# Kernel tuning notes

Measured on AMD Instinct MI355X. Metric: run time of the kernel, lower is better.

## Reference

```python
import jax, jax.numpy as jnp
import numpy as np

# ---- Mamba2 hyperparameters (from init_kwargs + mamba_ssm defaults) ----
D_MODEL = 1024
D_STATE = 64
D_CONV = 4
EXPAND = 2
HEADDIM = 64                       # mamba_ssm default
D_INNER = EXPAND * D_MODEL         # 2048
NHEADS = D_INNER // HEADDIM        # 32
CONV_DIM = D_INNER + 2 * D_STATE   # 2176 (ngroups=1)
D_IN_PROJ = 2 * D_INNER + 2 * D_STATE + NHEADS  # 4256
CHUNK = 64                         # SSD chunk length
EPS = 1e-5


def segsum(x):
    """Stable segment-sum: out[..., i, j] = sum_{k=j+1..i} x[..., k] for i>=j, else -inf."""
    T = x.shape[-1]
    cs = jnp.cumsum(x, axis=-1)
    ss = cs[..., :, None] - cs[..., None, :]
    mask = jnp.tril(jnp.ones((T, T), dtype=bool))
    return jnp.where(mask, ss, -jnp.inf)


def setup_inputs() -> dict:
    key = jax.random.key(0)
    ks = jax.random.split(key, 8)
    x = jax.random.normal(ks[0], (2, 2048, D_MODEL), dtype=jnp.float32)
    ln_w = jnp.ones((D_MODEL,), jnp.float32)
    ln_b = jnp.zeros((D_MODEL,), jnp.float32)
    in_proj_w = jax.random.normal(ks[1], (D_MODEL, D_IN_PROJ), jnp.float32) * 0.02
    conv_w = jax.random.normal(ks[2], (CONV_DIM, D_CONV), jnp.float32) * 0.2
    conv_b = jnp.zeros((CONV_DIM,), jnp.float32)
    dt_bias = jax.random.normal(ks[3], (NHEADS,), jnp.float32) * 0.5
    A_log = jnp.log(jax.random.uniform(ks[4], (NHEADS,), jnp.float32, 1.0, 16.0))
    D = jnp.ones((NHEADS,), jnp.float32)
    norm_w = jnp.ones((D_INNER,), jnp.float32)
    out_proj_w = jax.random.normal(ks[5], (D_INNER, D_MODEL), jnp.float32) * 0.02
    return {"x": x, "ln_w": ln_w, "ln_b": ln_b, "in_proj_w": in_proj_w,
            "conv_w": conv_w, "conv_b": conv_b, "dt_bias": dt_bias,
            "A_log": A_log, "D": D, "norm_w": norm_w, "out_proj_w": out_proj_w}


def reference(x, ln_w, ln_b, in_proj_w, conv_w, conv_b, dt_bias, A_log, D,
              norm_w, out_proj_w):
    b, l, _ = x.shape
    # ---- pre-norm (LayerNorm) ----
    mu = jnp.mean(x, -1, keepdims=True)
    var = jnp.mean((x - mu) ** 2, -1, keepdims=True)
    h = (x - mu) * jax.lax.rsqrt(var + EPS) * ln_w + ln_b

    # ---- input projection & split ----
    zxbcdt = h @ in_proj_w                                   # (b,l,4256)
    z, xBC, dt = jnp.split(zxbcdt, [D_INNER, D_INNER + CONV_DIM], axis=-1)

    # ---- causal depthwise conv1d + SiLU ----
    xp = jnp.pad(xBC, ((0, 0), (D_CONV - 1, 0), (0, 0)))
    xconv = sum(xp[:, k:k + l, :] * conv_w[:, k] for k in range(D_CONV)) + conv_b
    xBC = jax.nn.silu(xconv)
    xs, B, C = jnp.split(xBC, [D_INNER, D_INNER + D_STATE], axis=-1)

    dt = jax.nn.softplus(dt + dt_bias)                       # (b,l,h)
    A = -jnp.exp(A_log)                                      # (h,)
    X = xs.reshape(b, l, NHEADS, HEADDIM)                    # (b,l,h,p)

    # ---- SSD chunked selective scan ----
    c = l // CHUNK
    X_dt = X * dt[..., None]
    A_dt = dt * A                                            # (b,l,h)
    Xc = X_dt.reshape(b, c, CHUNK, NHEADS, HEADDIM)          # (b,c,T,h,p)
    Ac = A_dt.reshape(b, c, CHUNK, NHEADS).transpose(0, 3, 1, 2)  # (b,h,c,T)
    Bc = B.reshape(b, c, CHUNK, D_STATE)                     # (b,c,T,n)
    Cc = C.reshape(b, c, CHUNK, D_STATE)

    A_cs = jnp.cumsum(Ac, axis=-1)                           # (b,h,c,T)
    Lmat = jnp.exp(segsum(Ac))                               # (b,h,c,T,T)
    Y_diag = jnp.einsum("bcln,bcsn,bhcls,bcshp->bclhp", Cc, Bc, Lmat, Xc)

    decay_states = jnp.exp(A_cs[..., -1:] - A_cs)            # (b,h,c,T)
    states = jnp.einsum("bcln,bhcl,bclhp->bchpn", Bc, decay_states, Xc)

    A_last = jnp.pad(A_cs[..., -1], ((0, 0), (0, 0), (1, 0)))
    decay_chunk = jnp.exp(segsum(A_last))                    # (b,h,c+1,c+1)
    states = jnp.concatenate([jnp.zeros_like(states[:, :1]), states], axis=1)
    states = jnp.einsum("bhzc,bchpn->bzhpn", decay_chunk, states)[:, :-1]

    Y_off = jnp.einsum("bcln,bchpn,bhcl->bclhp", Cc, states, jnp.exp(A_cs))
    Y = (Y_diag + Y_off).reshape(b, l, NHEADS, HEADDIM)

    # ---- D skip, gated RMSNorm, output projection ----
    Y = Y + X * D[None, None, :, None]
    y = Y.reshape(b, l, D_INNER)
    y = y * jax.nn.silu(z)
    y = y * jax.lax.rsqrt(jnp.mean(y * y, -1, keepdims=True) + EPS) * norm_w
    out = y @ out_proj_w

    return x + out  # residual
```

## Files before the change

### kernel.cpp

```cpp
#include <hip/hip_runtime.h>
#include <hip/hip_bf16.h>

#define BATCH   2
#define SEQ     2048
#define DMODEL  1024
#define DINNER  2048
#define DSTATE  64
#define NHEADS  32
#define HEADDIM 64
#define CONVDIM 2176
#define DINPROJ 4256
#define NPAD    4352
#define NCHUNK  32
#define EPSF    1e-5f
#define SP      88
#define CDT     (CONVDIM + NHEADS)

typedef __bf16 bf16;
typedef bf16  bf16x4 __attribute__((ext_vector_type(4)));
typedef bf16  bf16x8 __attribute__((ext_vector_type(8)));
typedef float f32x4  __attribute__((ext_vector_type(4)));

__device__ __forceinline__ void gll16(const bf16* g, bf16* l) {
    __builtin_amdgcn_global_load_lds(
        (const __attribute__((address_space(1))) void*)g,
        (__attribute__((address_space(3))) void*)l, 16, 0, 0);
}

__global__ __launch_bounds__(256) void ln_kernel(
    const float* __restrict__ x, const float* __restrict__ w,
    const float* __restrict__ bv, bf16* __restrict__ h) {
    int row = blockIdx.x;
    const float* xr = x + (size_t)row * DMODEL;
    bf16* hr = h + (size_t)row * DMODEL;
    int t = threadIdx.x;
    float4 v = ((const float4*)xr)[t];
    float s  = v.x + v.y + v.z + v.w;
    float ss = v.x*v.x + v.y*v.y + v.z*v.z + v.w*v.w;
    for (int o = 32; o > 0; o >>= 1) { s += __shfl_down(s, o); ss += __shfl_down(ss, o); }
    __shared__ float red[2][4];
    int wid = t >> 6, lane = t & 63;
    if (lane == 0) { red[0][wid] = s; red[1][wid] = ss; }
    __syncthreads();
    if (t == 0) {
        float a = 0, b2 = 0;
        for (int i = 0; i < 4; i++) { a += red[0][i]; b2 += red[1][i]; }
        red[0][0] = a; red[1][0] = b2;
    }
    __syncthreads();
    float mean = red[0][0] * (1.f / DMODEL);
    float var  = red[1][0] * (1.f / DMODEL) - mean * mean;
    float rstd = rsqrtf(var + EPSF);
    for (int i = t; i < DMODEL; i += 256)
        hr[i] = (bf16)((xr[i] - mean) * rstd * w[i] + bv[i]);
}

__global__ __launch_bounds__(256) void cvt_w_both_kernel(
    const float* __restrict__ W1, const float* __restrict__ W2,
    bf16* __restrict__ Bt1, bf16* __restrict__ Bt2) {
    __shared__ float sm[32][33];
    int bid = blockIdx.x;
    const float* W; bf16* Bt; int K, N, NP, bx, by;
    if (bid < 4352) {
        W = W1; Bt = Bt1; K = 1024; N = 4256; NP = 4352;
        bx = bid % 136; by = bid / 136;
    } else {
        int b2 = bid - 4352;
        W = W2; Bt = Bt2; K = 2048; N = 1024; NP = 1024;
        bx = b2 % 32; by = b2 / 32;
    }
    int n0 = bx * 32, k0 = by * 32;
    int tx = threadIdx.x & 31, ty = threadIdx.x >> 5;
    for (int i = 0; i < 4; i++) {
        int k = k0 + ty + i * 8, n = n0 + tx;
        sm[ty + i * 8][tx] = (n < N) ? W[(size_t)k * N + n] : 0.f;
    }
    __syncthreads();
    for (int i = 0; i < 4; i++) {
        int n = n0 + ty + i * 8, k = k0 + tx;
        if (n < NP) Bt[(size_t)n * K + k] = (bf16)sm[tx][ty + i * 8];
    }
}

template<int BM, int BN, typename OUT_T>
__global__ __launch_bounds__(256) void gemm_bf16_pipe(
    const bf16* __restrict__ A, const bf16* __restrict__ Bt,
    OUT_T* __restrict__ C, int M, int N, int K,
    const float* __restrict__ resid) {
    constexpr int MR = BM / 32;
    constexpr int NR = BN / 32;
    __shared__ __align__(16) bf16 sA[2][BM * 32];
    __shared__ __align__(16) bf16 sB[2][BN * 32];
    int t = threadIdx.x;
    int lane = t & 63, w = t >> 6;
    int m0 = blockIdx.y * BM, n0 = blockIdx.x * BN;
    int wm = w >> 1, wn = w & 1;
    f32x4 acc[MR][NR] = {};
    int srow = w * 16 + (lane >> 2);
    int scol = (lane & 3) * 8;
    int fr = lane & 15;
    int fc = (lane >> 4) * 8;
    auto stage = [&](int buf, int k0) {
        #pragma unroll
        for (int i = 0; i < BM / 64; i++)
            gll16(&A[(size_t)(m0 + i * 64 + srow) * K + k0 + scol],
                  &sA[buf][(i * 64 + w * 16) * 32]);
        #pragma unroll
        for (int i = 0; i < BN / 64; i++)
            gll16(&Bt[(size_t)(n0 + i * 64 + srow) * K + k0 + scol],
                  &sB[buf][(i * 64 + w * 16) * 32]);
    };
    int nt = K / 32;
    stage(0, 0);
    __syncthreads();
    int cur = 0;
    for (int tt = 0; tt < nt; tt++) {
        if (tt + 1 < nt) stage(cur ^ 1, (tt + 1) * 32);
        bf16x8 af[MR], bfr[NR];
        #pragma unroll
        for (int i = 0; i < MR; i++)
            af[i] = *(const bf16x8*)&sA[cur][(wm * (BM/2) + i * 16 + fr) * 32 + fc];
        #pragma unroll
        for (int j = 0; j < NR; j++)
            bfr[j] = *(const bf16x8*)&sB[cur][(wn * (BN/2) + j * 16 + fr) * 32 + fc];
        #pragma unroll
        for (int i = 0; i < MR; i++)
            #pragma unroll
            for (int j = 0; j < NR; j++)
                acc[i][j] = __builtin_amdgcn_mfma_f32_16x16x32_bf16(
                    af[i], bfr[j], acc[i][j], 0, 0, 0);
        __syncthreads();
        cur ^= 1;
    }
    #pragma unroll
    for (int i = 0; i < MR; i++) {
        #pragma unroll
        for (int j = 0; j < NR; j++) {
            int col = n0 + wn * (BN/2) + j * 16 + (lane & 15);
            #pragma unroll
            for (int r = 0; r < 4; r++) {
                int row = m0 + wm * (BM/2) + i * 16 + (lane >> 4) * 4 + r;
                float v = acc[i][j][r];
                if (resid) v += resid[(size_t)row * N + col];
                C[(size_t)row * N + col] = (OUT_T)v;
            }
        }
    }
}

__global__ __launch_bounds__(256) void convdt_kernel(
    const bf16* __restrict__ zx, const float* __restrict__ cw,
    const float* __restrict__ cb, const float* __restrict__ dt_bias,
    bf16* __restrict__ xs, bf16* __restrict__ Bm, bf16* __restrict__ Cm,
    float* __restrict__ dtb) {
    int idx = blockIdx.x * 256 + threadIdx.x;
    int ch = idx % CDT;
    int bl = idx / CDT;
    if (ch >= CONVDIM) {
        int hh = ch - CONVDIM;
        float v = (float)zx[(size_t)bl * NPAD + DINNER + ch] + dt_bias[hh];
        dtb[bl * NHEADS + hh] = (v > 20.f) ? v : log1pf(expf(v));
        return;
    }
    int b = bl / SEQ, tt = bl % SEQ;
    float acc = cb[ch];
    #pragma unroll
    for (int k = 0; k < 4; k++) {
        int tp = tt - 3 + k;
        if (tp >= 0)
            acc += (float)zx[(size_t)(b * SEQ + tp) * NPAD + DINNER + ch] * cw[ch * 4 + k];
    }
    float s = acc / (1.f + expf(-acc));
    if (ch < DINNER)              xs[(size_t)bl * DINNER + ch] = (bf16)s;
    else if (ch < DINNER+DSTATE)  Bm[bl * DSTATE + (ch - DINNER)] = (bf16)s;
    else                          Cm[bl * DSTATE + (ch - DINNER - DSTATE)] = (bf16)s;
}

__global__ __launch_bounds__(256) void ssd_states_kernel(
    const bf16* __restrict__ xs, const bf16* __restrict__ Bm,
    const float* __restrict__ dtb, const float* __restrict__ A_log,
    bf16* __restrict__ states, float* __restrict__ Acs_g) {
    int blk = blockIdx.x;
    int hh = blk % NHEADS;
    int bc = blk / NHEADS;
    int c = bc % NCHUNK, b = bc / NCHUNK;
    __shared__ __align__(16) bf16 sXT[64 * SP];
    __shared__ __align__(16) bf16 sBT[64 * SP];
    __shared__ float dts[64], acs[64];
    int t = threadIdx.x;
    float Ah = -expf(A_log[hh]);
    if (t < 64) {
        float dv = dtb[(b * SEQ + c * 64 + t) * NHEADS + hh];
        float v = dv * Ah;
        #pragma unroll
        for (int o = 1; o < 64; o <<= 1) {
            float p = __shfl_up(v, o);
            if (t >= o) v += p;
        }
        dts[t] = dv; acs[t] = v;
        Acs_g[((b * NHEADS + hh) * NCHUNK + c) * 64 + t] = v;
    }
    __syncthreads();
    float alast = acs[63];
    {
        int l = t >> 2, c0 = (t & 3) * 16;
        int row = b * SEQ + c * 64 + l;
        float dl = dts[l];
        float wl = expf(alast - acs[l]);
        bf16x8 xv0 = *(const bf16x8*)&xs[(size_t)row * DINNER + hh * 64 + c0];
        bf16x8 xv1 = *(const bf16x8*)&xs[(size_t)row * DINNER + hh * 64 + c0 + 8];
        bf16x8 bv0 = *(const bf16x8*)&Bm[(size_t)row * DSTATE + c0];
        bf16x8 bv1 = *(const bf16x8*)&Bm[(size_t)row * DSTATE + c0 + 8];
        #pragma unroll
        for (int i = 0; i < 8; i++) {
            sXT[(c0 + i) * SP + l]     = (bf16)((float)xv0[i] * dl);
            sXT[(c0 + 8 + i) * SP + l] = (bf16)((float)xv1[i] * dl);
            sBT[(c0 + i) * SP + l]     = (bf16)((float)bv0[i] * wl);
            sBT[(c0 + 8 + i) * SP + l] = (bf16)((float)bv1[i] * wl);
        }
    }
    __syncthreads();
    int lane = t & 63, w = t >> 6;
    int wm = w >> 1, wn = w & 1;
    int fr = lane & 15, fc = (lane >> 4) * 8;
    f32x4 acc[2][2] = {};
    #pragma unroll
    for (int kk = 0; kk < 2; kk++) {
        bf16x8 a[2], bb[2];
        #pragma unroll
        for (int i = 0; i < 2; i++)
            a[i] = *(const bf16x8*)&sXT[(wm * 32 + i * 16 + fr) * SP + kk * 32 + fc];
        #pragma unroll
        for (int j = 0; j < 2; j++)
            bb[j] = *(const bf16x8*)&sBT[(wn * 32 + j * 16 + fr) * SP + kk * 32 + fc];
        #pragma unroll
        for (int i = 0; i < 2; i++)
            #pragma unroll
            for (int j = 0; j < 2; j++)
                acc[i][j] = __builtin_amdgcn_mfma_f32_16x16x32_bf16(
                    a[i], bb[j], acc[i][j], 0, 0, 0);
    }
    bf16* outp = states + (size_t)blk * 4096;
    #pragma unroll
    for (int i = 0; i < 2; i++)
        #pragma unroll
        for (int j = 0; j < 2; j++)
            #pragma unroll
            for (int r = 0; r < 4; r++)
                outp[(wm*32 + i*16 + (lane>>4)*4 + r) * 64 + wn*32 + j*16 + (lane&15)]
                    = (bf16)acc[i][j][r];
}

__global__ __launch_bounds__(256) void ssd_scan_kernel(
    bf16* __restrict__ states, const float* __restrict__ Acs_g) {
    int bid = blockIdx.x;
    int slice = bid & 3, bh = bid >> 2;
    int hh = bh % NHEADS, b = bh / NHEADS;
    int e0 = slice * 1024 + threadIdx.x * 4;
    bf16x4 loc[NCHUNK];
    float dec[NCHUNK];
    #pragma unroll
    for (int c = 0; c < NCHUNK; c++) {
        loc[c] = *(const bf16x4*)&states[(size_t)((b*NCHUNK+c)*NHEADS+hh)*4096 + e0];
        dec[c] = expf(Acs_g[((b*NHEADS+hh)*NCHUNK + c)*64 + 63]);
    }
    float S0 = 0.f, S1 = 0.f, S2 = 0.f, S3 = 0.f;
    #pragma unroll
    for (int c = 0; c < NCHUNK; c++) {
        bf16x4 l = loc[c];
        bf16x4 o; o[0] = (bf16)S0; o[1] = (bf16)S1; o[2] = (bf16)S2; o[3] = (bf16)S3;
        *(bf16x4*)&states[(size_t)((b*NCHUNK+c)*NHEADS+hh)*4096 + e0] = o;
        S0 = dec[c]*S0 + (float)l[0];
        S1 = dec[c]*S1 + (float)l[1];
        S2 = dec[c]*S2 + (float)l[2];
        S3 = dec[c]*S3 + (float)l[3];
    }
}

__global__ __launch_bounds__(256) void ssd_out_kernel(
    const bf16* __restrict__ xs, const bf16* __restrict__ Bm,
    const bf16* __restrict__ Cm, const float* __restrict__ dtb,
    const bf16* __restrict__ states, const float* __restrict__ Acs_g,
    const float* __restrict__ Dv, bf16* __restrict__ Y) {
    int blk = blockIdx.x;
    int hh = blk % NHEADS;
    int bc = blk / NHEADS;
    int c = bc % NCHUNK, b = bc / NCHUNK;
    __shared__ __align__(16) bf16 sC [64 * SP];
    __shared__ __align__(16) bf16 sBG[64 * SP];
    __shared__ __align__(16) bf16 sXS[64 * SP];
    __shared__ float acs[64], dts[64];
    int t = threadIdx.x;
    bf16x8 sreg0, sreg1;
    {
        const bf16* sp = states + (size_t)blk * 4096 + t * 16;
        sreg0 = *(const bf16x8*)&sp[0];
        sreg1 = *(const bf16x8*)&sp[8];
    }
    if (t < 64) {
        acs[t] = Acs_g[((b * NHEADS + hh) * NCHUNK + c) * 64 + t];
        dts[t] = dtb[(b * SEQ + c * 64 + t) * NHEADS + hh];
    }
    {
        int l = t >> 2, c0 = (t & 3) * 16;
        int row = b * SEQ + c * 64 + l;
        *(bf16x8*)&sC[l * SP + c0]      = *(const bf16x8*)&Cm[(size_t)row * DSTATE + c0];
        *(bf16x8*)&sC[l * SP + c0 + 8]  = *(const bf16x8*)&Cm[(size_t)row * DSTATE + c0 + 8];
        *(bf16x8*)&sBG[l * SP + c0]     = *(const bf16x8*)&Bm[(size_t)row * DSTATE + c0];
        *(bf16x8*)&sBG[l * SP + c0 + 8] = *(const bf16x8*)&Bm[(size_t)row * DSTATE + c0 + 8];
        bf16x8 xv0 = *(const bf16x8*)&xs[(size_t)row * DINNER + hh * 64 + c0];
        bf16x8 xv1 = *(const bf16x8*)&xs[(size_t)row * DINNER + hh * 64 + c0 + 8];
        #pragma unroll
        for (int i = 0; i < 8; i++) {
            sXS[(c0 + i) * SP + l]     = xv0[i];
            sXS[(c0 + 8 + i) * SP + l] = xv1[i];
        }
    }
    __syncthreads();
    int lane = t & 63, w = t >> 6;
    int wm = w >> 1, wn = w & 1;
    int fr = lane & 15, fc = (lane >> 4) * 8;
    f32x4 g[2][2] = {};
    #pragma unroll
    for (int kk = 0; kk < 2; kk++) {
        bf16x8 a[2], bb[2];
        #pragma unroll
        for (int i = 0; i < 2; i++)
            a[i] = *(const bf16x8*)&sC[(wm * 32 + i * 16 + fr) * SP + kk * 32 + fc];
        #pragma unroll
        for (int j = 0; j < 2; j++)
            bb[j] = *(const bf16x8*)&sBG[(wn * 32 + j * 16 + fr) * SP + kk * 32 + fc];
        #pragma unroll
        for (int i = 0; i < 2; i++)
            #pragma unroll
            for (int j = 0; j < 2; j++)
                g[i][j] = __builtin_amdgcn_mfma_f32_16x16x32_bf16(a[i], bb[j], g[i][j], 0, 0, 0);
    }
    __syncthreads();
    #pragma unroll
    for (int i = 0; i < 2; i++) {
        #pragma unroll
        for (int j = 0; j < 2; j++) {
            int s = wn * 32 + j * 16 + (lane & 15);
            #pragma unroll
            for (int r = 0; r < 4; r++) {
                int l = wm * 32 + i * 16 + (lane >> 4) * 4 + r;
                float val = (s <= l) ? g[i][j][r] * expf(acs[l] - acs[s]) * dts[s] : 0.f;
                sBG[l * SP + s] = (bf16)val;
            }
        }
    }
    __syncthreads();
    f32x4 yd[2][2] = {};
    #pragma unroll
    for (int kk = 0; kk < 2; kk++) {
        bf16x8 a[2], bb[2];
        #pragma unroll
        for (int i = 0; i < 2; i++)
            a[i] = *(const bf16x8*)&sBG[(wm * 32 + i * 16 + fr) * SP + kk * 32 + fc];
        #pragma unroll
        for (int j = 0; j < 2; j++)
            bb[j] = *(const bf16x8*)&sXS[(wn * 32 + j * 16 + fr) * SP + kk * 32 + fc];
        #pragma unroll
        for (int i = 0; i < 2; i++)
            #pragma unroll
            for (int j = 0; j < 2; j++)
                yd[i][j] = __builtin_amdgcn_mfma_f32_16x16x32_bf16(a[i], bb[j], yd[i][j], 0, 0, 0);
    }
    float xk[2][2][4];
    #pragma unroll
    for (int i = 0; i < 2; i++)
        #pragma unroll
        for (int j = 0; j < 2; j++) {
            int p = wn * 32 + j * 16 + (lane & 15);
            #pragma unroll
            for (int r = 0; r < 4; r++) {
                int l = wm * 32 + i * 16 + (lane >> 4) * 4 + r;
                xk[i][j][r] = (float)sXS[p * SP + l];
            }
        }
    __syncthreads();
    {
        int p = t >> 2, n0 = (t & 3) * 16;
        *(bf16x8*)&sXS[p * SP + n0]     = sreg0;
        *(bf16x8*)&sXS[p * SP + n0 + 8] = sreg1;
    }
    __syncthreads();
    f32x4 yo[2][2] = {};
    #pragma unroll
    for (int kk = 0; kk < 2; kk++) {
        bf16x8 a[2], bb[2];
        #pragma unroll
        for (int i = 0; i < 2; i++)
            a[i] = *(const bf16x8*)&sC[(wm * 32 + i * 16 + fr) * SP + kk * 32 + fc];
        #pragma unroll
        for (int j = 0; j < 2; j++)
            bb[j] = *(const bf16x8*)&sXS[(wn * 32 + j * 16 + fr) * SP + kk * 32 + fc];
        #pragma unroll
        for (int i = 0; i < 2; i++)
            #pragma unroll
            for (int j = 0; j < 2; j++)
                yo[i][j] = __builtin_amdgcn_mfma_f32_16x16x32_bf16(a[i], bb[j], yo[i][j], 0, 0, 0);
    }
    float Dh = Dv[hh];
    #pragma unroll
    for (int i = 0; i < 2; i++) {
        #pragma unroll
        for (int j = 0; j < 2; j++) {
            int p = wn * 32 + j * 16 + (lane & 15);
            #pragma unroll
            for (int r = 0; r < 4; r++) {
                int l = wm * 32 + i * 16 + (lane >> 4) * 4 + r;
                int row = b * SEQ + c * 64 + l;
                Y[(size_t)row * DINNER + hh * 64 + p] =
                    (bf16)(yd[i][j][r] + expf(acs[l]) * yo[i][j][r] + Dh * xk[i][j][r]);
            }
        }
    }
}

__global__ __launch_bounds__(256) void rms_kernel(
    const bf16* __restrict__ Y, const bf16* __restrict__ zx,
    const float* __restrict__ nw, bf16* __restrict__ yn) {
    int row = blockIdx.x;
    const bf16* yr = Y + (size_t)row * DINNER;
    const bf16* zr = zx + (size_t)row * NPAD;
    bf16* outr = yn + (size_t)row * DINNER;
    int t = threadIdx.x;
    float vals[8];
    float ss = 0.f;
    #pragma unroll
    for (int i = 0; i < 8; i++) {
        int idx = t + i * 256;
        float z = (float)zr[idx];
        float v = (float)yr[idx] * (z / (1.f + expf(-z)));
        vals[i] = v;
        ss += v * v;
    }
    for (int o = 32; o > 0; o >>= 1) ss += __shfl_down(ss, o);
    __shared__ float red[4];
    int wid = t >> 6, lane = t & 63;
    if (lane == 0) red[wid] = ss;
    __syncthreads();
    if (t == 0) { float a = 0; for (int i = 0; i < 4; i++) a += red[i]; red[0] = a; }
    __syncthreads();
    float r = rsqrtf(red[0] * (1.f / DINNER) + EPSF);
    #pragma unroll
    for (int i = 0; i < 8; i++) {
        int idx = t + i * 256;
        outr[idx] = (bf16)(vals[i] * r * nw[idx]);
    }
}

extern "C" void kernel_launch(void* const* d_in, const int* in_sizes, int n_in,
                              void* d_out, int out_size, void* d_ws, size_t ws_size,
                              hipStream_t stream) {
    const float* x          = (const float*)d_in[0];
    const float* ln_w       = (const float*)d_in[1];
    const float* ln_b       = (const float*)d_in[2];
    const float* in_proj_w  = (const float*)d_in[3];
    const float* conv_w     = (const float*)d_in[4];
    const float* conv_b     = (const float*)d_in[5];
    const float* dt_bias    = (const float*)d_in[6];
    const float* A_log      = (const float*)d_in[7];
    const float* Dv         = (const float*)d_in[8];
    const float* norm_w     = (const float*)d_in[9];
    const float* out_proj_w = (const float*)d_in[10];
    float* out = (float*)d_out;

    char* ws = (char*)d_ws;
    size_t off = 0;
    auto alloc = [&](size_t bytes) { char* p = ws + off; off += (bytes + 255) & ~(size_t)255; return p; };
    bf16*  h_bf  = (bf16*) alloc((size_t)4096 * DMODEL * 2);
    bf16*  zx    = (bf16*) alloc((size_t)4096 * NPAD * 2);
    bf16*  xs    = (bf16*) alloc((size_t)4096 * DINNER * 2);
    bf16*  states= (bf16*) alloc((size_t)2048 * 4096 * 2);
    bf16*  Yb    = (bf16*) alloc((size_t)4096 * DINNER * 2);
    bf16*  Bt1   = (bf16*) alloc((size_t)NPAD * DMODEL * 2);
    bf16*  Bt2   = (bf16*) alloc((size_t)DMODEL * DINNER * 2);
    float* dtb   = (float*)alloc((size_t)4096 * NHEADS * 4);
    float* Acs   = (float*)alloc((size_t)2 * NHEADS * NCHUNK * 64 * 4);
    bf16* Bm = h_bf;
    bf16* Cm = h_bf + (size_t)4096 * DSTATE;
    bf16* yn = xs;

    cvt_w_both_kernel<<<4352 + 2048, 256, 0, stream>>>(in_proj_w, out_proj_w, Bt1, Bt2);

    ln_kernel<<<BATCH * SEQ, 256, 0, stream>>>(x, ln_w, ln_b, h_bf);

    {
        dim3 g(NPAD / 128, (BATCH * SEQ) / 128);
        gemm_bf16_pipe<128, 128, bf16><<<g, 256, 0, stream>>>(
            h_bf, Bt1, zx, BATCH * SEQ, NPAD, DMODEL, nullptr);
    }

    convdt_kernel<<<(BATCH * SEQ * CDT) / 256, 256, 0, stream>>>(
        zx, conv_w, conv_b, dt_bias, xs, Bm, Cm, dtb);

    ssd_states_kernel<<<BATCH * NCHUNK * NHEADS, 256, 0, stream>>>(
        xs, Bm, dtb, A_log, states, Acs);

    ssd_scan_kernel<<<BATCH * NHEADS * 4, 256, 0, stream>>>(states, Acs);

    ssd_out_kernel<<<BATCH * NCHUNK * NHEADS, 256, 0, stream>>>(
        xs, Bm, Cm, dtb, states, Acs, Dv, Yb);

    rms_kernel<<<BATCH * SEQ, 256, 0, stream>>>(Yb, zx, norm_w, yn);

    {
        dim3 g(DMODEL / 64, (BATCH * SEQ) / 128);
        gemm_bf16_pipe<128, 64, float><<<g, 256, 0, stream>>>(
            yn, Bt2, out, BATCH * SEQ, DMODEL, DINNER, x);
    }
}
```

Before: 206.9 us.

## Triple-buffer GEMM loads with explicit vmcnt waits and fuse prep kernels

```diff
diff --git a/kernel.cpp b/kernel.cpp
--- a/kernel.cpp
+++ b/kernel.cpp
@@ -21,76 +21,86 @@
 typedef bf16  bf16x8 __attribute__((ext_vector_type(8)));
 typedef float f32x4  __attribute__((ext_vector_type(4)));
 
+template<int V> struct IC { static constexpr int value = V; };
+
 __device__ __forceinline__ void gll16(const bf16* g, bf16* l) {
     __builtin_amdgcn_global_load_lds(
         (const __attribute__((address_space(1))) void*)g,
         (__attribute__((address_space(3))) void*)l, 16, 0, 0);
 }
 
-__global__ __launch_bounds__(256) void ln_kernel(
-    const float* __restrict__ x, const float* __restrict__ w,
-    const float* __restrict__ bv, bf16* __restrict__ h) {
-    int row = blockIdx.x;
+template<int VM> __device__ __forceinline__ void vmwait() {
+    if constexpr (VM == 0) asm volatile("s_waitcnt vmcnt(0)" ::: "memory");
+    if constexpr (VM == 3) asm volatile("s_waitcnt vmcnt(3)" ::: "memory");
+    if constexpr (VM == 4) asm volatile("s_waitcnt vmcnt(4)" ::: "memory");
+    if constexpr (VM == 6) asm volatile("s_waitcnt vmcnt(6)" ::: "memory");
+    if constexpr (VM == 8) asm volatile("s_waitcnt vmcnt(8)" ::: "memory");
+}
+
+__global__ __launch_bounds__(256) void pre_kernel(
+    const float* __restrict__ x, const float* __restrict__ lw,
+    const float* __restrict__ lb, bf16* __restrict__ h,
+    const float* __restrict__ W1, const float* __restrict__ W2,
+    bf16* __restrict__ Bt1, bf16* __restrict__ Bt2) {
+    __shared__ float sm[32][33];
+    int bid = blockIdx.x;
+    int t = threadIdx.x;
+    if (bid < 6400) {
+        const float* W; bf16* Bt; int K, N, NP, bx, by;
+        if (bid < 4352) {
+            W = W1; Bt = Bt1; K = 1024; N = 4256; NP = 4352;
+            bx = bid % 136; by = bid / 136;
+        } else {
+            int b2 = bid - 4352;
+            W = W2; Bt = Bt2; K = 2048; N = 1024; NP = 1024;
+            bx = b2 % 32; by = b2 / 32;
+        }
+        int n0 = bx * 32, k0 = by * 32;
+        int tx = t & 31, ty = t >> 5;
+        for (int i = 0; i < 4; i++) {
+            int k = k0 + ty + i * 8, n = n0 + tx;
+            sm[ty + i * 8][tx] = (n < N) ? W[(size_t)k * N + n] : 0.f;
+        }
+        __syncthreads();
+        for (int i = 0; i < 4; i++) {
+            int n = n0 + ty + i * 8, k = k0 + tx;
+            if (n < NP) Bt[(size_t)n * K + k] = (bf16)sm[tx][ty + i * 8];
+        }
+        return;
+    }
+    int row = bid - 6400;
     const float* xr = x + (size_t)row * DMODEL;
     bf16* hr = h + (size_t)row * DMODEL;
-    int t = threadIdx.x;
     float4 v = ((const float4*)xr)[t];
     float s  = v.x + v.y + v.z + v.w;
     float ss = v.x*v.x + v.y*v.y + v.z*v.z + v.w*v.w;
     for (int o = 32; o > 0; o >>= 1) { s += __shfl_down(s, o); ss += __shfl_down(ss, o); }
-    __shared__ float red[2][4];
     int wid = t >> 6, lane = t & 63;
-    if (lane == 0) { red[0][wid] = s; red[1][wid] = ss; }
+    if (lane == 0) { sm[0][wid] = s; sm[1][wid] = ss; }
     __syncthreads();
     if (t == 0) {
         float a = 0, b2 = 0;
-        for (int i = 0; i < 4; i++) { a += red[0][i]; b2 += red[1][i]; }
-        red[0][0] = a; red[1][0] = b2;
-    }
-    __syncthreads();
-    float mean = red[0][0] * (1.f / DMODEL);
-    float var  = red[1][0] * (1.f / DMODEL) - mean * mean;
+        for (int i = 0; i < 4; i++) { a += sm[0][i]; b2 += sm[1][i]; }
+        sm[0][0] = a; sm[1][0] = b2;
+    }
+    __syncthreads();
+    float mean = sm[0][0] * (1.f / DMODEL);
+    float var  = sm[1][0] * (1.f / DMODEL) - mean * mean;
     float rstd = rsqrtf(var + EPSF);
     for (int i = t; i < DMODEL; i += 256)
-        hr[i] = (bf16)((xr[i] - mean) * rstd * w[i] + bv[i]);
-}
-
-__global__ __launch_bounds__(256) void cvt_w_both_kernel(
-    const float* __restrict__ W1, const float* __restrict__ W2,
-    bf16* __restrict__ Bt1, bf16* __restrict__ Bt2) {
-    __shared__ float sm[32][33];
-    int bid = blockIdx.x;
-    const float* W; bf16* Bt; int K, N, NP, bx, by;
-    if (bid < 4352) {
-        W = W1; Bt = Bt1; K = 1024; N = 4256; NP = 4352;
-        bx = bid % 136; by = bid / 136;
-    } else {
-        int b2 = bid - 4352;
-        W = W2; Bt = Bt2; K = 2048; N = 1024; NP = 1024;
-        bx = b2 % 32; by = b2 / 32;
-    }
-    int n0 = bx * 32, k0 = by * 32;
-    int tx = threadIdx.x & 31, ty = threadIdx.x >> 5;
-    for (int i = 0; i < 4; i++) {
-        int k = k0 + ty + i * 8, n = n0 + tx;
-        sm[ty + i * 8][tx] = (n < N) ? W[(size_t)k * N + n] : 0.f;
-    }
-    __syncthreads();
-    for (int i = 0; i < 4; i++) {
-        int n = n0 + ty + i * 8, k = k0 + tx;
-        if (n < NP) Bt[(size_t)n * K + k] = (bf16)sm[tx][ty + i * 8];
-    }
+        hr[i] = (bf16)((xr[i] - mean) * rstd * lw[i] + lb[i]);
 }
 
 template<int BM, int BN, typename OUT_T>
-__global__ __launch_bounds__(256) void gemm_bf16_pipe(
+__global__ __launch_bounds__(256) void gemm_bf16_pipe3(
     const bf16* __restrict__ A, const bf16* __restrict__ Bt,
     OUT_T* __restrict__ C, int M, int N, int K,
     const float* __restrict__ resid) {
     constexpr int MR = BM / 32;
     constexpr int NR = BN / 32;
-    __shared__ __align__(16) bf16 sA[2][BM * 32];
-    __shared__ __align__(16) bf16 sB[2][BN * 32];
+    constexpr int LPT = BM / 64 + BN / 64;
+    __shared__ __align__(16) bf16 sA[3][BM * 32];
+    __shared__ __align__(16) bf16 sB[3][BN * 32];
     int t = threadIdx.x;
     int lane = t & 63, w = t >> 6;
     int m0 = blockIdx.y * BM, n0 = blockIdx.x * BN;
@@ -111,27 +121,35 @@
                   &sB[buf][(i * 64 + w * 16) * 32]);
     };
     int nt = K / 32;
-    stage(0, 0);
-    __syncthreads();
-    int cur = 0;
-    for (int tt = 0; tt < nt; tt++) {
-        if (tt + 1 < nt) stage(cur ^ 1, (tt + 1) * 32);
+    stage(0, 0); stage(1, 32); stage(2, 64);
+    int tt = 0;
+    auto iter = [&](auto vmtag) {
+        constexpr int VM = decltype(vmtag)::value;
+        vmwait<VM>();
+        __builtin_amdgcn_s_barrier();
+        int buf = tt % 3;
         bf16x8 af[MR], bfr[NR];
         #pragma unroll
         for (int i = 0; i < MR; i++)
-            af[i] = *(const bf16x8*)&sA[cur][(wm * (BM/2) + i * 16 + fr) * 32 + fc];
+            af[i] = *(const bf16x8*)&sA[buf][(wm * (BM/2) + i * 16 + fr) * 32 + fc];
         #pragma unroll
         for (int j = 0; j < NR; j++)
-            bfr[j] = *(const bf16x8*)&sB[cur][(wn * (BN/2) + j * 16 + fr) * 32 + fc];
+            bfr[j] = *(const bf16x8*)&sB[buf][(wn * (BN/2) + j * 16 + fr) * 32 + fc];
+        asm volatile("s_waitcnt lgkmcnt(0)" ::: "memory");
+        __builtin_amdgcn_sched_barrier(0);
+        __builtin_amdgcn_s_barrier();
+        if (tt + 3 < nt) stage(buf, (tt + 3) * 32);
         #pragma unroll
         for (int i = 0; i < MR; i++)
             #pragma unroll
             for (int j = 0; j < NR; j++)
                 acc[i][j] = __builtin_amdgcn_mfma_f32_16x16x32_bf16(
                     af[i], bfr[j], acc[i][j], 0, 0, 0);
-        __syncthreads();
-        cur ^= 1;
-    }
+        tt++;
+    };
+    for (; tt < nt - 2; ) iter(IC<2 * LPT>{});
+    iter(IC<LPT>{});
+    iter(IC<0>{});
     #pragma unroll
     for (int i = 0; i < MR; i++) {
         #pragma unroll
@@ -484,13 +502,12 @@
     bf16* Cm = h_bf + (size_t)4096 * DSTATE;
     bf16* yn = xs;
 
-    cvt_w_both_kernel<<<4352 + 2048, 256, 0, stream>>>(in_proj_w, out_proj_w, Bt1, Bt2);
-
-    ln_kernel<<<BATCH * SEQ, 256, 0, stream>>>(x, ln_w, ln_b, h_bf);
+    pre_kernel<<<6400 + 4096, 256, 0, stream>>>(
+        x, ln_w, ln_b, h_bf, in_proj_w, out_proj_w, Bt1, Bt2);
 
     {
         dim3 g(NPAD / 128, (BATCH * SEQ) / 128);
-        gemm_bf16_pipe<128, 128, bf16><<<g, 256, 0, stream>>>(
+        gemm_bf16_pipe3<128, 128, bf16><<<g, 256, 0, stream>>>(
             h_bf, Bt1, zx, BATCH * SEQ, NPAD, DMODEL, nullptr);
     }
 
@@ -509,7 +526,7 @@
 
     {
         dim3 g(DMODEL / 64, (BATCH * SEQ) / 128);
-        gemm_bf16_pipe<128, 64, float><<<g, 256, 0, stream>>>(
+        gemm_bf16_pipe3<128, 64, float><<<g, 256, 0, stream>>>(
             yn, Bt2, out, BATCH * SEQ, DMODEL, DINNER, x);
     }
 }
```

Result: faster. 198.2 us (-4.2%).
